# Optimization experiments

Hardware: AMD Instinct MI355X
Metric: run time of the kernel (lower is better)

Reference implementation:

```python
import jax, jax.numpy as jnp
import numpy as np

N_NODES = 100000
N_EDGES = 800000
D_MODEL = 128
N_HEAD = 8
LN_EPS = 1e-6


def setup_inputs() -> dict:
    key = jax.random.key(0)
    ks = jax.random.split(key, 6)
    embeds = jax.random.normal(ks[0], (N_NODES, D_MODEL), dtype=jnp.float32)
    # xavier_uniform bound for square [d, d] matrix: sqrt(6 / (d + d))
    bound = float(np.sqrt(6.0 / (D_MODEL + D_MODEL)))
    qW = jax.random.uniform(ks[1], (D_MODEL, D_MODEL), minval=-bound, maxval=bound, dtype=jnp.float32)
    kW = jax.random.uniform(ks[2], (D_MODEL, D_MODEL), minval=-bound, maxval=bound, dtype=jnp.float32)
    vW = jax.random.uniform(ks[3], (D_MODEL, D_MODEL), minval=-bound, maxval=bound, dtype=jnp.float32)
    ln_gamma = jnp.ones((D_MODEL,), dtype=jnp.float32)
    ln_beta = jnp.zeros((D_MODEL,), dtype=jnp.float32)
    edge_index = jax.random.randint(ks[4], (2, N_EDGES), 0, N_NODES, dtype=jnp.int64)
    return {"embeds": embeds, "qW": qW, "kW": kW, "vW": vW,
            "ln_gamma": ln_gamma, "ln_beta": ln_beta, "edge_index": edge_index}


def reference(embeds, qW, kW, vW, ln_gamma, ln_beta, edge_index):
    rows = edge_index[0]  # destination (softmax segment) indices, [E]
    cols = edge_index[1]  # source indices, [E]
    n_nodes, d_model = embeds.shape
    n_edges = rows.shape[0]
    head = N_HEAD
    d_head = d_model // head

    row_e = embeds[rows]                      # [E, d]
    col_e = embeds[cols]                      # [E, d]
    q = (row_e @ qW).reshape(n_edges, head, d_head)
    k = (col_e @ kW).reshape(n_edges, head, d_head)
    v = (col_e @ vW).reshape(n_edges, head, d_head)

    att = jnp.einsum('ehd,ehd->eh', q, k)     # [E, h]
    att = jnp.clip(att, -10.0, 10.0)
    exp_att = jnp.exp(att)

    # segment-softmax normalization over destination node
    att_norm = jax.ops.segment_sum(exp_att, rows, num_segments=n_nodes)  # [N, h]
    att = exp_att / (att_norm[rows] + 1e-8)   # [E, h]

    res_e = (att[:, :, None] * v).reshape(n_edges, d_model)              # [E, d]
    res = jax.ops.segment_sum(res_e, rows, num_segments=n_nodes)         # [N, d]
    res = res + embeds

    # LayerNorm(eps=1e-6) over last dim
    mean = jnp.mean(res, axis=-1, keepdims=True)
    var = jnp.mean((res - mean) ** 2, axis=-1, keepdims=True)
    out = (res - mean) * jax.lax.rsqrt(var + LN_EPS) * ln_gamma + ln_beta
    return out
```

## Files before the change

### kernel.cpp

```cpp
#include <hip/hip_runtime.h>
#include <hip/hip_bf16.h>

#define N_NODES 100000
#define N_EDGES 800000
#define D 128
#define NH 8
#define NB ((N_NODES + 255) / 256)

typedef __hip_bfloat16 bf16;
typedef __bf16 bf16x8 __attribute__((ext_vector_type(8)));
typedef float  f32x4  __attribute__((ext_vector_type(4)));

__device__ __forceinline__ unsigned short f2bu(float x) {
    bf16 b = __float2bfloat16(x);
    return *reinterpret_cast<unsigned short*>(&b);
}
__device__ __forceinline__ float bu2f(unsigned short u) {
    return __uint_as_float(((unsigned)u) << 16);
}
__device__ __forceinline__ float bfe0(unsigned u) { return __uint_as_float(u << 16); }
__device__ __forceinline__ float bfe1(unsigned u) { return __uint_as_float(u & 0xffff0000u); }

union frag_u { unsigned short u[8]; bf16x8 v; };

__global__ __launch_bounds__(256) void wf_prep(
    const float* __restrict__ Wq, const float* __restrict__ Wk, const float* __restrict__ Wv,
    unsigned short* __restrict__ Wf)
{
    int t = blockIdx.x * 256 + threadIdx.x;
    if (t >= 3 * 32 * 64) return;
    int lane = t & 63;
    int ct   = (t >> 6) & 31;
    int mat  = t >> 11;
    const float* W = (mat == 0) ? Wq : (mat == 1) ? Wk : Wv;
    int c  = ct >> 3, tt = ct & 7;
    int n  = tt * 16 + (lane & 15);
    int kb = c * 32 + (lane >> 4) * 8;
    unsigned short* dst = Wf + (size_t)mat * 32768 + (size_t)ct * 1024 + (size_t)lane * 8;
#pragma unroll
    for (int j = 0; j < 8; ++j) {
        float w  = W[(size_t)(kb + j) * D + n];
        unsigned short hb = f2bu(w);
        float lo = w - bu2f(hb);
        dst[j]       = hb;
        dst[512 + j] = f2bu(lo);
    }
}

__global__ __launch_bounds__(256) void qkv_mfma(
    const float* __restrict__ E, const unsigned short* __restrict__ Wf,
    bf16* __restrict__ Q, bf16* __restrict__ K, bf16* __restrict__ V)
{
    __shared__ unsigned short obuf[4][16 * 136];
    const int wave = threadIdx.x >> 6;
    const int lane = threadIdx.x & 63;
    const int r0 = (blockIdx.x * 4 + wave) * 16;
    if (r0 >= N_NODES) return;

    const int am = lane & 15;
    const int aq = lane >> 4;

    const float* erow = E + (size_t)(r0 + am) * D + aq * 8;
    frag_u ahi[4], alo[4];
#pragma unroll
    for (int c = 0; c < 4; ++c) {
        float4 e0 = *reinterpret_cast<const float4*>(erow + c * 32);
        float4 e1 = *reinterpret_cast<const float4*>(erow + c * 32 + 4);
        float ef[8] = {e0.x, e0.y, e0.z, e0.w, e1.x, e1.y, e1.z, e1.w};
#pragma unroll
        for (int j = 0; j < 8; ++j) {
            unsigned short hb = f2bu(ef[j]);
            ahi[c].u[j] = hb;
            alo[c].u[j] = f2bu(ef[j] - bu2f(hb));
        }
    }

    bf16* const Os[3] = {Q, K, V};
    unsigned short* ob = obuf[wave];
    const unsigned short* wfl = Wf + (size_t)lane * 8;

#pragma unroll
    for (int mat = 0; mat < 3; ++mat) {
        f32x4 acc[8];
#pragma unroll
        for (int t = 0; t < 8; ++t) acc[t] = (f32x4){0.f, 0.f, 0.f, 0.f};

        const unsigned short* wfm = wfl + (size_t)mat * 32768;
#pragma unroll
        for (int c = 0; c < 4; ++c) {
#pragma unroll
            for (int t = 0; t < 8; ++t) {
                const unsigned short* bp = wfm + (size_t)(c * 8 + t) * 1024;
                bf16x8 bhi = *reinterpret_cast<const bf16x8*>(bp);
                bf16x8 blo = *reinterpret_cast<const bf16x8*>(bp + 512);
                acc[t] = __builtin_amdgcn_mfma_f32_16x16x32_bf16(alo[c].v, bhi, acc[t], 0, 0, 0);
                acc[t] = __builtin_amdgcn_mfma_f32_16x16x32_bf16(ahi[c].v, blo, acc[t], 0, 0, 0);
                acc[t] = __builtin_amdgcn_mfma_f32_16x16x32_bf16(ahi[c].v, bhi, acc[t], 0, 0, 0);
            }
        }

#pragma unroll
        for (int t = 0; t < 8; ++t) {
#pragma unroll
            for (int r = 0; r < 4; ++r)
                ob[(aq * 4 + r) * 136 + t * 16 + am] = f2bu(acc[t][r]);
        }
        const int row = lane >> 2, c4 = lane & 3;
        const uint4* src = reinterpret_cast<const uint4*>(ob + row * 136 + c4 * 32);
        uint4 d0 = src[0], d1 = src[1], d2 = src[2], d3 = src[3];
        uint4* dst = reinterpret_cast<uint4*>(Os[mat] + (size_t)(r0 + row) * D + c4 * 32);
        dst[0] = d0; dst[1] = d1; dst[2] = d2; dst[3] = d3;
    }
}

__global__ __launch_bounds__(256) void hist_kernel(
    const int* __restrict__ rows, int* __restrict__ counts)
{
    int e = blockIdx.x * 256 + threadIdx.x;
    if (e < N_EDGES) atomicAdd(&counts[rows[e]], 1);
}

__global__ __launch_bounds__(256) void scan_block(
    const int* __restrict__ counts, int* __restrict__ scanned, int* __restrict__ block_sums)
{
    __shared__ int s[256];
    int tid = threadIdx.x;
    int i = blockIdx.x * 256 + tid;
    int v = (i < N_NODES) ? counts[i] : 0;
    s[tid] = v;
    __syncthreads();
#pragma unroll
    for (int off = 1; off < 256; off <<= 1) {
        int t = (tid >= off) ? s[tid - off] : 0;
        __syncthreads();
        s[tid] += t;
        __syncthreads();
    }
    if (i < N_NODES) scanned[i] = s[tid] - v;
    if (tid == 255) block_sums[blockIdx.x] = s[255];
}

__global__ __launch_bounds__(512) void scan_tops(int* __restrict__ block_sums)
{
    __shared__ int s[512];
    int tid = threadIdx.x;
    int v = (tid < NB) ? block_sums[tid] : 0;
    s[tid] = v;
    __syncthreads();
#pragma unroll
    for (int off = 1; off < 512; off <<= 1) {
        int t = (tid >= off) ? s[tid - off] : 0;
        __syncthreads();
        s[tid] += t;
        __syncthreads();
    }
    if (tid < NB) block_sums[tid] = s[tid] - v;
}

__global__ __launch_bounds__(256) void scan_add(
    int* __restrict__ scanned, const int* __restrict__ block_sums, int* __restrict__ cursor)
{
    int i = blockIdx.x * 256 + threadIdx.x;
    if (i < N_NODES) {
        int o = scanned[i] + block_sums[blockIdx.x];
        scanned[i] = o;
        cursor[i]  = o;
    }
}

__global__ __launch_bounds__(256) void scatter_kernel(
    const int* __restrict__ rows, const int* __restrict__ cols,
    int* __restrict__ cursor, int* __restrict__ csr_cols)
{
    int e = blockIdx.x * 256 + threadIdx.x;
    if (e < N_EDGES) {
        int pos = atomicAdd(&cursor[rows[e]], 1);
        csr_cols[pos] = cols[e];
    }
}

__global__ __launch_bounds__(256) void fused_node(
    const bf16* __restrict__ Qb, const bf16* __restrict__ Kb, const bf16* __restrict__ Vb,
    const int* __restrict__ offsets, const int* __restrict__ counts,
    const int* __restrict__ csr_cols,
    const float* __restrict__ emb,
    const float* __restrict__ gamma, const float* __restrict__ beta,
    float* __restrict__ out)
{
    int n = blockIdx.x * 4 + (threadIdx.x >> 6);
    int lane = threadIdx.x & 63;
    if (n >= N_NODES) return;

    unsigned qu = *reinterpret_cast<const unsigned*>(Qb + (size_t)n * D + lane * 2);
    float q0 = bfe0(qu), q1 = bfe1(qu);

    int start = offsets[n];
    int cnt   = counts[n];

    const bf16* kbase = Kb + lane * 2;
    const bf16* vbase = Vb + lane * 2;

    float acc0 = 0.f, acc1 = 0.f, nrm = 0.f;
    for (int base = 0; base < cnt; base += 64) {
        int m = cnt - base; if (m > 64) m = 64;
        int myc = (base + lane < cnt) ? csr_cols[start + base + lane] : 0;
        int j = 0;
        for (; j + 1 < m; j += 2) {
            int c0 = __shfl(myc, j, 64);
            int c1 = __shfl(myc, j + 1, 64);
            unsigned ku0 = *reinterpret_cast<const unsigned*>(kbase + (size_t)c0 * D);
            unsigned vu0 = *reinterpret_cast<const unsigned*>(vbase + (size_t)c0 * D);
            unsigned ku1 = *reinterpret_cast<const unsigned*>(kbase + (size_t)c1 * D);
            unsigned vu1 = *reinterpret_cast<const unsigned*>(vbase + (size_t)c1 * D);
            float p0 = q0 * bfe0(ku0) + q1 * bfe1(ku0);
            float p1 = q0 * bfe0(ku1) + q1 * bfe1(ku1);
            p0 += __shfl_xor(p0, 1, 64);
            p1 += __shfl_xor(p1, 1, 64);
            p0 += __shfl_xor(p0, 2, 64);
            p1 += __shfl_xor(p1, 2, 64);
            p0 += __shfl_xor(p0, 4, 64);
            p1 += __shfl_xor(p1, 4, 64);
            float s0 = __expf(fminf(fmaxf(p0, -10.f), 10.f));
            float s1 = __expf(fminf(fmaxf(p1, -10.f), 10.f));
            nrm  += s0 + s1;
            acc0 += s0 * bfe0(vu0) + s1 * bfe0(vu1);
            acc1 += s0 * bfe1(vu0) + s1 * bfe1(vu1);
        }
        if (j < m) {
            int c0 = __shfl(myc, j, 64);
            unsigned ku0 = *reinterpret_cast<const unsigned*>(kbase + (size_t)c0 * D);
            unsigned vu0 = *reinterpret_cast<const unsigned*>(vbase + (size_t)c0 * D);
            float p0 = q0 * bfe0(ku0) + q1 * bfe1(ku0);
            p0 += __shfl_xor(p0, 1, 64);
            p0 += __shfl_xor(p0, 2, 64);
            p0 += __shfl_xor(p0, 4, 64);
            float s0 = __expf(fminf(fmaxf(p0, -10.f), 10.f));
            nrm  += s0;
            acc0 += s0 * bfe0(vu0);
            acc1 += s0 * bfe1(vu0);
        }
    }

    float w = 1.f / (nrm + 1e-8f);
    float2 e2 = *reinterpret_cast<const float2*>(emb + (size_t)n * D + lane * 2);
    float x0 = acc0 * w + e2.x;
    float x1 = acc1 * w + e2.y;

    float ssum = x0 + x1;
#pragma unroll
    for (int off = 32; off; off >>= 1) ssum += __shfl_xor(ssum, off, 64);
    float mean = ssum * (1.0f / 128.0f);
    float d0 = x0 - mean, d1 = x1 - mean;
    float var = d0 * d0 + d1 * d1;
#pragma unroll
    for (int off = 32; off; off >>= 1) var += __shfl_xor(var, off, 64);
    float rs = rsqrtf(var * (1.0f / 128.0f) + 1e-6f);

    float2 g2 = *reinterpret_cast<const float2*>(gamma + lane * 2);
    float2 b2 = *reinterpret_cast<const float2*>(beta + lane * 2);
    float2 o2 = make_float2(d0 * rs * g2.x + b2.x, d1 * rs * g2.y + b2.y);
    *reinterpret_cast<float2*>(out + (size_t)n * D + lane * 2) = o2;
}

extern "C" void kernel_launch(void* const* d_in, const int* in_sizes, int n_in,
                              void* d_out, int out_size, void* d_ws, size_t ws_size,
                              hipStream_t stream)
{
    const float* emb   = (const float*)d_in[0];
    const float* qW    = (const float*)d_in[1];
    const float* kW    = (const float*)d_in[2];
    const float* vW    = (const float*)d_in[3];
    const float* gamma = (const float*)d_in[4];
    const float* beta  = (const float*)d_in[5];
    const int*   eidx  = (const int*)d_in[6];
    const int*   rows  = eidx;
    const int*   cols  = eidx + N_EDGES;
    float* out = (float*)d_out;

    const size_t ND = (size_t)N_NODES * D;
    bf16* Qb = (bf16*)d_ws;
    bf16* Kb = Qb + ND;
    bf16* Vb = Kb + ND;
    int* counts     = (int*)(Vb + ND);
    int* offsets    = counts + N_NODES;
    int* cursor     = offsets + N_NODES;
    int* block_sums = cursor + N_NODES;
    int* csr_cols   = block_sums + 512;
    unsigned short* Wf = (unsigned short*)(csr_cols + N_EDGES);

    hipMemsetAsync(counts, 0, (size_t)N_NODES * sizeof(int), stream);

    wf_prep<<<24, 256, 0, stream>>>(qW, kW, vW, Wf);
    qkv_mfma<<<(N_NODES + 63) / 64, 256, 0, stream>>>(emb, Wf, Qb, Kb, Vb);

    hist_kernel<<<(N_EDGES + 255) / 256, 256, 0, stream>>>(rows, counts);
    scan_block<<<NB, 256, 0, stream>>>(counts, offsets, block_sums);
    scan_tops<<<1, 512, 0, stream>>>(block_sums);
    scan_add<<<NB, 256, 0, stream>>>(offsets, block_sums, cursor);
    scatter_kernel<<<(N_EDGES + 255) / 256, 256, 0, stream>>>(rows, cols, cursor, csr_cols);

    fused_node<<<(N_NODES + 3) / 4, 256, 0, stream>>>(
        Qb, Kb, Vb, offsets, counts, csr_cols, emb, gamma, beta, out);
}
```

Before: 338.3 us.

## Stage QKV weights in LDS and compute two row tiles per wave

The QKV projection kernel copies each half of a weight matrix's bf16 hi/lo fragments into shared memory once per block. Each wave now computes 32 rows (two 16-row tiles), so every loaded B fragment is reused for two A tiles. This is meant to cut redundant global/L2 weight traffic per node. In exchange it adds block-wide barriers, doubles the accumulator and A-fragment registers, and halves the grid size, which may lower occupancy.

```diff
diff --git a/kernel.cpp b/kernel.cpp
--- a/kernel.cpp
+++ b/kernel.cpp
@@ -51,65 +51,94 @@
     const float* __restrict__ E, const unsigned short* __restrict__ Wf,
     bf16* __restrict__ Q, bf16* __restrict__ K, bf16* __restrict__ V)
 {
-    __shared__ unsigned short obuf[4][16 * 136];
-    const int wave = threadIdx.x >> 6;
-    const int lane = threadIdx.x & 63;
-    const int r0 = (blockIdx.x * 4 + wave) * 16;
-    if (r0 >= N_NODES) return;
+    __shared__ unsigned short bsh[16384];
+    const int tid  = threadIdx.x;
+    const int wave = tid >> 6;
+    const int lane = tid & 63;
+    const int r0w  = blockIdx.x * 128 + wave * 32;
 
     const int am = lane & 15;
     const int aq = lane >> 4;
 
-    const float* erow = E + (size_t)(r0 + am) * D + aq * 8;
-    frag_u ahi[4], alo[4];
-#pragma unroll
-    for (int c = 0; c < 4; ++c) {
-        float4 e0 = *reinterpret_cast<const float4*>(erow + c * 32);
-        float4 e1 = *reinterpret_cast<const float4*>(erow + c * 32 + 4);
-        float ef[8] = {e0.x, e0.y, e0.z, e0.w, e1.x, e1.y, e1.z, e1.w};
-#pragma unroll
-        for (int j = 0; j < 8; ++j) {
-            unsigned short hb = f2bu(ef[j]);
-            ahi[c].u[j] = hb;
-            alo[c].u[j] = f2bu(ef[j] - bu2f(hb));
+    frag_u ahi[2][4], alo[2][4];
+#pragma unroll
+    for (int rt = 0; rt < 2; ++rt) {
+        int row = r0w + rt * 16 + am;
+        if (row >= N_NODES) row = N_NODES - 1;
+        const float* erow = E + (size_t)row * D + aq * 8;
+#pragma unroll
+        for (int c = 0; c < 4; ++c) {
+            float4 e0 = *reinterpret_cast<const float4*>(erow + c * 32);
+            float4 e1 = *reinterpret_cast<const float4*>(erow + c * 32 + 4);
+            float ef[8] = {e0.x, e0.y, e0.z, e0.w, e1.x, e1.y, e1.z, e1.w};
+#pragma unroll
+            for (int j = 0; j < 8; ++j) {
+                unsigned short hb = f2bu(ef[j]);
+                ahi[rt][c].u[j] = hb;
+                alo[rt][c].u[j] = f2bu(ef[j] - bu2f(hb));
+            }
         }
     }
 
     bf16* const Os[3] = {Q, K, V};
-    unsigned short* ob = obuf[wave];
-    const unsigned short* wfl = Wf + (size_t)lane * 8;
 
 #pragma unroll
     for (int mat = 0; mat < 3; ++mat) {
-        f32x4 acc[8];
-#pragma unroll
-        for (int t = 0; t < 8; ++t) acc[t] = (f32x4){0.f, 0.f, 0.f, 0.f};
-
-        const unsigned short* wfm = wfl + (size_t)mat * 32768;
-#pragma unroll
-        for (int c = 0; c < 4; ++c) {
+        f32x4 acc[8][2];
+#pragma unroll
+        for (int t = 0; t < 8; ++t)
+#pragma unroll
+            for (int rt = 0; rt < 2; ++rt)
+                acc[t][rt] = (f32x4){0.f, 0.f, 0.f, 0.f};
+
+        const unsigned short* wm = Wf + (size_t)mat * 32768;
+
+#pragma unroll
+        for (int half = 0; half < 2; ++half) {
+            __syncthreads();
+            const uint4* src = reinterpret_cast<const uint4*>(wm + half * 16384);
+            uint4* dstv = reinterpret_cast<uint4*>(bsh);
+#pragma unroll
+            for (int k = 0; k < 8; ++k)
+                dstv[k * 256 + tid] = src[k * 256 + tid];
+            __syncthreads();
+
 #pragma unroll
             for (int t = 0; t < 8; ++t) {
-                const unsigned short* bp = wfm + (size_t)(c * 8 + t) * 1024;
-                bf16x8 bhi = *reinterpret_cast<const bf16x8*>(bp);
-                bf16x8 blo = *reinterpret_cast<const bf16x8*>(bp + 512);
-                acc[t] = __builtin_amdgcn_mfma_f32_16x16x32_bf16(alo[c].v, bhi, acc[t], 0, 0, 0);
-                acc[t] = __builtin_amdgcn_mfma_f32_16x16x32_bf16(ahi[c].v, blo, acc[t], 0, 0, 0);
-                acc[t] = __builtin_amdgcn_mfma_f32_16x16x32_bf16(ahi[c].v, bhi, acc[t], 0, 0, 0);
+#pragma unroll
+                for (int cc = 0; cc < 2; ++cc) {
+                    const unsigned short* bp = bsh + (cc * 8 + t) * 1024 + lane * 8;
+                    bf16x8 bhi = *reinterpret_cast<const bf16x8*>(bp);
+                    bf16x8 blo = *reinterpret_cast<const bf16x8*>(bp + 512);
+                    const int c = half * 2 + cc;
+#pragma unroll
+                    for (int rt = 0; rt < 2; ++rt) {
+                        acc[t][rt] = __builtin_amdgcn_mfma_f32_16x16x32_bf16(alo[rt][c].v, bhi, acc[t][rt], 0, 0, 0);
+                        acc[t][rt] = __builtin_amdgcn_mfma_f32_16x16x32_bf16(ahi[rt][c].v, blo, acc[t][rt], 0, 0, 0);
+                        acc[t][rt] = __builtin_amdgcn_mfma_f32_16x16x32_bf16(ahi[rt][c].v, bhi, acc[t][rt], 0, 0, 0);
+                    }
+                }
             }
         }
-
-#pragma unroll
-        for (int t = 0; t < 8; ++t) {
-#pragma unroll
-            for (int r = 0; r < 4; ++r)
-                ob[(aq * 4 + r) * 136 + t * 16 + am] = f2bu(acc[t][r]);
-        }
-        const int row = lane >> 2, c4 = lane & 3;
-        const uint4* src = reinterpret_cast<const uint4*>(ob + row * 136 + c4 * 32);
-        uint4 d0 = src[0], d1 = src[1], d2 = src[2], d3 = src[3];
-        uint4* dst = reinterpret_cast<uint4*>(Os[mat] + (size_t)(r0 + row) * D + c4 * 32);
-        dst[0] = d0; dst[1] = d1; dst[2] = d2; dst[3] = d3;
+        __syncthreads();
+
+        unsigned short* ob = bsh + wave * 2176;
+#pragma unroll
+        for (int rt = 0; rt < 2; ++rt) {
+#pragma unroll
+            for (int t = 0; t < 8; ++t)
+#pragma unroll
+                for (int r = 0; r < 4; ++r)
+                    ob[(aq * 4 + r) * 136 + t * 16 + am] = f2bu(acc[t][rt][r]);
+            const int row = lane >> 2, c4 = lane & 3;
+            int grow = r0w + rt * 16 + row;
+            if (grow < N_NODES) {
+                const uint4* srcb = reinterpret_cast<const uint4*>(ob + row * 136 + c4 * 32);
+                uint4 d0 = srcb[0], d1 = srcb[1], d2 = srcb[2], d3 = srcb[3];
+                uint4* dst = reinterpret_cast<uint4*>(Os[mat] + (size_t)grow * D + c4 * 32);
+                dst[0] = d0; dst[1] = d1; dst[2] = d2; dst[3] = d3;
+            }
+        }
     }
 }
 
@@ -291,7 +320,7 @@
     hipMemsetAsync(counts, 0, (size_t)N_NODES * sizeof(int), stream);
 
     wf_prep<<<24, 256, 0, stream>>>(qW, kW, vW, Wf);
-    qkv_mfma<<<(N_NODES + 63) / 64, 256, 0, stream>>>(emb, Wf, Qb, Kb, Vb);
+    qkv_mfma<<<(N_NODES + 127) / 128, 256, 0, stream>>>(emb, Wf, Qb, Kb, Vb);
 
     hist_kernel<<<(N_EDGES + 255) / 256, 256, 0, stream>>>(rows, counts);
     scan_block<<<NB, 256, 0, stream>>>(counts, offsets, block_sums);
```

New measurement: 315.3 us. 6.8% less time.
